# Optimization experiments

Measured on AMD Instinct MI355X. Metric: run time of the kernel, lower is better.

## Reference

```python
import jax, jax.numpy as jnp
import numpy as np

T, N, XD, H, Z, E = 6, 4096, 64, 256, 128, 131072


def setup_inputs() -> dict:
    key = jax.random.key(0)
    ks = jax.random.split(key, 16)
    f32 = jnp.float32
    def rn(k, shp):
        return jax.random.normal(k, shp, f32)
    def gl(k, shp):  # glorot-ish init, scaled by fan_in
        return jax.random.normal(k, shp, f32) * np.float32(1.0 / np.sqrt(shp[-2]))
    return {
        "x": rn(ks[0], (T, N, XD)),
        "edges": jax.random.randint(ks[1], (T, 2, E), 0, N, dtype=jnp.int32),
        "eps": rn(ks[2], (T, N, Z)),
        "drop_u": jax.random.uniform(ks[3], (T, N, Z), f32),
        "phi_x_w": gl(ks[4], (XD, H)), "phi_x_b": jnp.zeros((H,), f32),
        "phi_z_w": gl(ks[5], (Z, H)), "phi_z_b": jnp.zeros((H,), f32),
        "enc_w": gl(ks[6], (2 * H, H)),
        "enc_mu_w": gl(ks[7], (H, Z)),
        "enc_lv_w": gl(ks[8], (H, Z)),
        "prior_w": gl(ks[9], (H, H)), "prior_b": jnp.zeros((H,), f32),
        "prior_mu_w": gl(ks[10], (H, Z)), "prior_mu_b": jnp.zeros((Z,), f32),
        "prior_lv_w": gl(ks[11], (H, Z)), "prior_lv_b": jnp.zeros((Z,), f32),
        "gru_wx": gl(ks[12], (4, 2 * H, H)),  # gates i,f,o,c; x-side GCN weights
        "gru_wh": gl(ks[13], (4, H, H)),      # gates i,f,o,c; h-side GCN weights
    }


def reference(x, edges, eps, drop_u, phi_x_w, phi_x_b, phi_z_w, phi_z_b,
              enc_w, enc_mu_w, enc_lv_w, prior_w, prior_b,
              prior_mu_w, prior_mu_b, prior_lv_w, prior_lv_b,
              gru_wx, gru_wh):
    T_, N_, _ = x.shape
    H_ = phi_x_w.shape[1]
    h = jnp.zeros((N_, H_), x.dtype)
    c = jnp.zeros((N_, H_), x.dtype)
    loop = jnp.arange(N_, dtype=edges.dtype)
    enc_mus, prior_mus = [], []
    dec_t = None
    for t in range(T_):  # fixed small T; edge structure differs per step
        row = jnp.concatenate([edges[t, 0], loop])  # add self loops
        col = jnp.concatenate([edges[t, 1], loop])
        deg = jax.ops.segment_sum(jnp.ones(row.shape, x.dtype), row, num_segments=N_)
        dinv = jnp.where(deg > 0, jax.lax.rsqrt(deg), jnp.zeros((), x.dtype))
        norm = (dinv[row] * dinv[col])[:, None]

        def gcn(xx, W):
            # GCNConv: xW, gather at col, scale by sym-norm, scatter-add at row
            return jax.ops.segment_sum(norm * (xx @ W)[col], row, num_segments=N_)

        phi_x_t = jax.nn.relu(x[t] @ phi_x_w + phi_x_b)
        enc_t = jax.nn.relu(gcn(jnp.concatenate([phi_x_t, h], axis=1), enc_w))
        enc_mu_t = gcn(enc_t, enc_mu_w)
        enc_std_t = jax.nn.softplus(gcn(enc_t, enc_lv_w))
        prior_t = jax.nn.relu(h @ prior_w + prior_b)
        prior_mu_t = prior_t @ prior_mu_w + prior_mu_b
        _prior_std_t = jax.nn.softplus(prior_t @ prior_lv_w + prior_lv_b)  # computed as in original, unused in returns
        z_t = eps[t] * enc_std_t + enc_mu_t  # original: eps.mul(logvar).add_(mu)
        phi_z_t = jax.nn.relu(z_t @ phi_z_w + phi_z_b)
        # InnerProductDecoder with dropout(p=0.5, training=True), identity act
        z_drop = jnp.where(drop_u[t] < 0.5, z_t * 2.0, jnp.zeros((), x.dtype))
        dec_t = z_drop @ z_drop.T  # [N, N]
        # graph-LSTM step (n_layer = 1)
        xin = jnp.concatenate([phi_x_t, phi_z_t], axis=1)  # [N, 2H]
        gi = jax.nn.sigmoid(gcn(xin, gru_wx[0]) + gcn(h, gru_wh[0]))
        gf = jax.nn.sigmoid(gcn(xin, gru_wx[1]) + gcn(h, gru_wh[1]))
        go = jax.nn.sigmoid(gcn(xin, gru_wx[2]) + gcn(h, gru_wh[2]))
        ct = jnp.tanh(gcn(xin, gru_wx[3]) + gcn(h, gru_wh[3]))
        c_new = gf * h + gi * ct    # faithful to original: F_g * h[i] (not c)
        h_new = go * jnp.tanh(c)    # faithful to original: uses old c[i]
        h, c = h_new, c_new
        enc_mus.append(enc_mu_t)
        prior_mus.append(prior_mu_t)
    return jnp.stack(enc_mus), jnp.stack(prior_mus), h[None], dec_t
```

## Files before the change

### kernel.cpp

```cpp
#include <hip/hip_runtime.h>
#include <math.h>

#define T_  6
#define NN  4096
#define XD_ 64
#define H_  256
#define ZZ  128
#define EE  131072

typedef unsigned short u16;
typedef __attribute__((ext_vector_type(8))) short short8;
typedef __attribute__((ext_vector_type(8))) unsigned short u16x8;
typedef __attribute__((ext_vector_type(4))) float f32x4;

__device__ __forceinline__ float bf2f(u16 u) { return __uint_as_float(((unsigned)u) << 16); }
__device__ __forceinline__ u16 f2bf(float f) {
    unsigned x = __float_as_uint(f);
    return (u16)((x + 0x7FFFu + ((x >> 16) & 1u)) >> 16);
}

__global__ void k_deg(const int* __restrict__ edges, int* __restrict__ degcnt) {
    int t = blockIdx.y;
    int e = blockIdx.x * 256 + threadIdx.x;
    const int* rows = edges + (size_t)t * 2 * EE;
    atomicAdd(&degcnt[t * NN + rows[e]], 1);
}

__global__ void k_scan_dinv(const int* __restrict__ degcnt_all,
                            int* __restrict__ row_start_all,
                            int* __restrict__ cursor_all,
                            float* __restrict__ dinv_all) {
    __shared__ int sbuf[1024];
    int tt = blockIdx.x;
    const int* degcnt = degcnt_all + tt * NN;
    int* row_start = row_start_all + tt * (NN + 1);
    int* cursor = cursor_all + tt * NN;
    float* dinv = dinv_all + tt * NN;
    int t = threadIdx.x;
    int b = t * 4;
    int v0 = degcnt[b + 0], v1 = degcnt[b + 1], v2 = degcnt[b + 2], v3 = degcnt[b + 3];
    dinv[b + 0] = rsqrtf((float)(v0 + 1));
    dinv[b + 1] = rsqrtf((float)(v1 + 1));
    dinv[b + 2] = rsqrtf((float)(v2 + 1));
    dinv[b + 3] = rsqrtf((float)(v3 + 1));
    int s = v0 + v1 + v2 + v3;
    sbuf[t] = s;
    __syncthreads();
    for (int off = 1; off < 1024; off <<= 1) {
        int x = sbuf[t];
        int y = (t >= off) ? sbuf[t - off] : 0;
        __syncthreads();
        sbuf[t] = x + y;
        __syncthreads();
    }
    int excl = sbuf[t] - s;
    int r0 = excl, r1 = excl + v0, r2 = r1 + v1, r3 = r2 + v2;
    row_start[b + 0] = r0; cursor[b + 0] = r0;
    row_start[b + 1] = r1; cursor[b + 1] = r1;
    row_start[b + 2] = r2; cursor[b + 2] = r2;
    row_start[b + 3] = r3; cursor[b + 3] = r3;
    if (t == 1023) row_start[NN] = r3 + v3;
}

__global__ void k_scatter(const int* __restrict__ edges,
                          int* __restrict__ cursor, const float* __restrict__ dinv,
                          int* __restrict__ col_idx, float* __restrict__ val,
                          const float* __restrict__ pm0, float* __restrict__ out_pm) {
    int idx = blockIdx.x * 256 + threadIdx.x;
    if (idx < T_ * EE) {
        int t = idx >> 17, e = idx & (EE - 1);
        const int* rows = edges + (size_t)t * 2 * EE;
        const int* cols = rows + EE;
        int r = rows[e], cc = cols[e];
        int pos = atomicAdd(&cursor[t * NN + r], 1);
        col_idx[(size_t)t * EE + pos] = cc;
        val[(size_t)t * EE + pos] = dinv[t * NN + r] * dinv[t * NN + cc];
        return;
    }
    idx -= T_ * EE;
    if (idx < NN * ZZ / 4) {
        int j4 = idx & 31;
        ((float4*)out_pm)[idx] = *(const float4*)(pm0 + j4 * 4);
    }
}

__device__ __forceinline__ void sp_row_wave(const u16* __restrict__ Y,
                                            const int* __restrict__ row_start,
                                            const int* __restrict__ col_idx,
                                            const float* __restrict__ val,
                                            const float* __restrict__ dinv,
                                            u16* __restrict__ outp, int ldo, int r) {
    int lane = threadIdx.x & 63;
    int half = lane >> 5;
    int cg2 = lane & 31;
    int s0 = row_start[r], s1 = row_start[r + 1];
    float a[8] = {0.f, 0.f, 0.f, 0.f, 0.f, 0.f, 0.f, 0.f};
    for (int base = s0; base < s1; base += 64) {
        int n = s1 - base; if (n > 64) n = 64;
        int cl = 0; float vl = 0.f;
        if (base + lane < s1) { cl = col_idx[base + lane]; vl = val[base + lane]; }
        for (int e = 0; e < n; e += 8) {
            int e0 = e + half, e1 = e + 2 + half, e2 = e + 4 + half, e3 = e + 6 + half;
            int cc0 = __shfl(cl, e0);
            float v0 = (e0 < n) ? __shfl(vl, e0) : 0.f;
            int cc1 = __shfl(cl, e1);
            float v1 = (e1 < n) ? __shfl(vl, e1) : 0.f;
            int cc2 = __shfl(cl, e2);
            float v2 = (e2 < n) ? __shfl(vl, e2) : 0.f;
            int cc3 = __shfl(cl, e3);
            float v3 = (e3 < n) ? __shfl(vl, e3) : 0.f;
            u16x8 y0 = *(const u16x8*)(Y + (size_t)cc0 * H_ + cg2 * 8);
            u16x8 y1 = *(const u16x8*)(Y + (size_t)cc1 * H_ + cg2 * 8);
            u16x8 y2 = *(const u16x8*)(Y + (size_t)cc2 * H_ + cg2 * 8);
            u16x8 y3 = *(const u16x8*)(Y + (size_t)cc3 * H_ + cg2 * 8);
#pragma unroll
            for (int j = 0; j < 8; ++j) a[j] += v0 * bf2f(y0[j]);
#pragma unroll
            for (int j = 0; j < 8; ++j) a[j] += v1 * bf2f(y1[j]);
#pragma unroll
            for (int j = 0; j < 8; ++j) a[j] += v2 * bf2f(y2[j]);
#pragma unroll
            for (int j = 0; j < 8; ++j) a[j] += v3 * bf2f(y3[j]);
        }
    }
#pragma unroll
    for (int j = 0; j < 8; ++j) a[j] += __shfl_xor(a[j], 32);
    if (half == 0) {
        float dr = dinv[r], sc = dr * dr;
        u16x8 ys = *(const u16x8*)(Y + (size_t)r * H_ + cg2 * 8);
        u16x8 o;
#pragma unroll
        for (int j = 0; j < 8; ++j) o[j] = f2bf(a[j] + sc * bf2f(ys[j]));
        *(u16x8*)(outp + (size_t)r * ldo + cg2 * 8) = o;
    }
}

__global__ void k_spmm(const u16* __restrict__ Y1,
                       const int* __restrict__ row_start_all, const int* __restrict__ col_idx_all,
                       const float* __restrict__ val_all, const float* __restrict__ dinv_all,
                       u16* __restrict__ out1, int ldo,
                       long long sY, long long sO) {
    int t = blockIdx.y;
    int w = threadIdx.x >> 6;
    sp_row_wave(Y1 + (size_t)t * sY, row_start_all + (size_t)t * (NN + 1),
                col_idx_all + (size_t)t * EE, val_all + (size_t)t * EE,
                dinv_all + (size_t)t * NN, out1 + (size_t)t * sO, ldo,
                blockIdx.x * 4 + w);
}

template<int MF>
__device__ __forceinline__ void mm_core(const u16* __restrict__ A, int lda,
                                        const u16* __restrict__ BT, int ldbt, int K,
                                        int row0, int col0,
                                        f32x4 acc[MF][MF], char* smem) {
    constexpr int TILE = MF * 32;
    u16* As = (u16*)smem;
    u16* Bs = As + TILE * 64;
    const int lane = threadIdx.x & 63;
    const int w = threadIdx.x >> 6;
    const int wr = (w >> 1) * (TILE / 2);
    const int wc = (w & 1) * (TILE / 2);

    int gRow[MF], gCol[MF];
#pragma unroll
    for (int i = 0; i < MF; ++i) {
        int G = (w * MF + i) * 64 + lane;
        int r = G >> 3;
        gRow[i] = r;
        gCol[i] = ((G & 7) ^ (r & 7)) << 3;
    }

    for (int k0 = 0; k0 < K; k0 += 64) {
#pragma unroll
        for (int i = 0; i < MF; ++i) {
            const u16* sa = A + (size_t)(row0 + gRow[i]) * lda + k0 + gCol[i];
            __builtin_amdgcn_global_load_lds(
                (const __attribute__((address_space(1))) void*)sa,
                (__attribute__((address_space(3))) void*)(As + (w * MF + i) * 512), 16, 0, 0);
            const u16* sb = BT + (size_t)(col0 + gRow[i]) * ldbt + k0 + gCol[i];
            __builtin_amdgcn_global_load_lds(
                (const __attribute__((address_space(1))) void*)sb,
                (__attribute__((address_space(3))) void*)(Bs + (w * MF + i) * 512), 16, 0, 0);
        }
        __syncthreads();
#pragma unroll
        for (int kk = 0; kk < 2; ++kk) {
            short8 a[MF], b[MF];
#pragma unroll
            for (int mf = 0; mf < MF; ++mf) {
                int r = wr + mf * 16 + (lane & 15);
                int off = (r * 128 + kk * 64 + (lane >> 4) * 16) ^ ((r & 7) << 4);
                a[mf] = *(const short8*)((const char*)As + off);
            }
#pragma unroll
            for (int nf = 0; nf < MF; ++nf) {
                int r = wc + nf * 16 + (lane & 15);
                int off = (r * 128 + kk * 64 + (lane >> 4) * 16) ^ ((r & 7) << 4);
                b[nf] = *(const short8*)((const char*)Bs + off);
            }
#pragma unroll
            for (int mf = 0; mf < MF; ++mf)
#pragma unroll
                for (int nf = 0; nf < MF; ++nf)
                    acc[mf][nf] = __builtin_amdgcn_mfma_f32_16x16x32_bf16(
                        a[mf], b[nf], acc[mf][nf], 0, 0, 0);
        }
        __syncthreads();
    }
}

__device__ __forceinline__ void mm_core32(const u16* __restrict__ A, int lda,
                                          const u16* __restrict__ BT, int ldbt, int K,
                                          int row0, int col0,
                                          f32x4 acc[2], char* smem) {
    u16* As = (u16*)smem;
    u16* Bs = As + 32 * 64;
    const int lane = threadIdx.x & 63;
    const int w = threadIdx.x >> 6;
    const int wr = (w >> 1) * 16;
    const int wc = (w & 1) * 32;

    int aR, aC;
    { int G = w * 64 + lane; int r = G >> 3; aR = r; aC = ((G & 7) ^ (r & 7)) << 3; }
    int bR[2], bC[2];
#pragma unroll
    for (int i = 0; i < 2; ++i) {
        int G = (w * 2 + i) * 64 + lane; int r = G >> 3;
        bR[i] = r; bC[i] = ((G & 7) ^ (r & 7)) << 3;
    }

    for (int k0 = 0; k0 < K; k0 += 64) {
        const u16* sa = A + (size_t)(row0 + aR) * lda + k0 + aC;
        __builtin_amdgcn_global_load_lds(
            (const __attribute__((address_space(1))) void*)sa,
            (__attribute__((address_space(3))) void*)(As + w * 512), 16, 0, 0);
#pragma unroll
        for (int i = 0; i < 2; ++i) {
            const u16* sb = BT + (size_t)(col0 + bR[i]) * ldbt + k0 + bC[i];
            __builtin_amdgcn_global_load_lds(
                (const __attribute__((address_space(1))) void*)sb,
                (__attribute__((address_space(3))) void*)(Bs + (w * 2 + i) * 512), 16, 0, 0);
        }
        __syncthreads();
#pragma unroll
        for (int kk = 0; kk < 2; ++kk) {
            short8 a, b[2];
            {
                int r = wr + (lane & 15);
                int off = (r * 128 + kk * 64 + (lane >> 4) * 16) ^ ((r & 7) << 4);
                a = *(const short8*)((const char*)As + off);
            }
#pragma unroll
            for (int nf = 0; nf < 2; ++nf) {
                int r = wc + nf * 16 + (lane & 15);
                int off = (r * 128 + kk * 64 + (lane >> 4) * 16) ^ ((r & 7) << 4);
                b[nf] = *(const short8*)((const char*)Bs + off);
            }
            acc[0] = __builtin_amdgcn_mfma_f32_16x16x32_bf16(a, b[0], acc[0], 0, 0, 0);
            acc[1] = __builtin_amdgcn_mfma_f32_16x16x32_bf16(a, b[1], acc[1], 0, 0, 0);
        }
        __syncthreads();
    }
}

__device__ __forceinline__ void zacc2(f32x4 acc[2][2]) {
#pragma unroll
    for (int i = 0; i < 2; ++i)
#pragma unroll
        for (int j = 0; j < 2; ++j) acc[i][j] = f32x4{0.f, 0.f, 0.f, 0.f};
}

__device__ __forceinline__ void epi_bf16relu(f32x4 acc[2][2], u16* __restrict__ C,
                                             int ldc, int row0, int col0,
                                             const float* __restrict__ bias) {
    const int lane = threadIdx.x & 63, w = threadIdx.x >> 6;
    const int wr = (w >> 1) * 32, wc = (w & 1) * 32;
    const int ci = lane & 15, ri = (lane >> 4) * 4;
#pragma unroll
    for (int mf = 0; mf < 2; ++mf)
#pragma unroll
        for (int nf = 0; nf < 2; ++nf) {
            int row = row0 + wr + mf * 16 + ri;
            int col = col0 + wc + nf * 16 + ci;
            float bv = bias ? bias[col] : 0.f;
#pragma unroll
            for (int i = 0; i < 4; ++i)
                C[(size_t)(row + i) * ldc + col] = f2bf(fmaxf(acc[mf][nf][i] + bv, 0.f));
        }
}

__device__ __forceinline__ void epi32_bf16relu(f32x4 acc[2], u16* __restrict__ C,
                                               int ldc, int row0, int col0,
                                               const float* __restrict__ bias) {
    const int lane = threadIdx.x & 63, w = threadIdx.x >> 6;
    const int wr = (w >> 1) * 16, wc = (w & 1) * 32;
    const int ci = lane & 15, ri = (lane >> 4) * 4;
#pragma unroll
    for (int nf = 0; nf < 2; ++nf) {
        int row = row0 + wr + ri;
        int col = col0 + wc + nf * 16 + ci;
        float bv = bias ? bias[col] : 0.f;
#pragma unroll
        for (int i = 0; i < 4; ++i)
            C[(size_t)(row + i) * ldc + col] = f2bf(fmaxf(acc[nf][i] + bv, 0.f));
    }
}

__device__ __forceinline__ void epi_f32b(f32x4 acc[2][2], float* __restrict__ C,
                                         int ldc, int row0, int col0,
                                         const float* __restrict__ bias) {
    const int lane = threadIdx.x & 63, w = threadIdx.x >> 6;
    const int wr = (w >> 1) * 32, wc = (w & 1) * 32;
    const int ci = lane & 15, ri = (lane >> 4) * 4;
#pragma unroll
    for (int mf = 0; mf < 2; ++mf)
#pragma unroll
        for (int nf = 0; nf < 2; ++nf) {
            int row = row0 + wr + mf * 16 + ri;
            int col = col0 + wc + nf * 16 + ci;
            float bv = bias[col];
#pragma unroll
            for (int i = 0; i < 4; ++i)
                C[(size_t)(row + i) * ldc + col] = acc[mf][nf][i] + bv;
        }
}

template<int MF>
__launch_bounds__(256)
__global__ void k_mm(const u16* __restrict__ A, int lda,
                     const u16* __restrict__ BT, int ldbt, int K,
                     float* __restrict__ C0, int ldc0,
                     u16* __restrict__ C1, int ldc1,
                     const float* __restrict__ bias, int act) {
    constexpr int TILE = MF * 32;
    __shared__ alignas(16) char smem[TILE * 64 * 4];

    const int lane = threadIdx.x & 63;
    const int w = threadIdx.x >> 6;
    const int row0 = blockIdx.y * TILE;
    const int col0 = blockIdx.x * TILE;
    const int wr = (w >> 1) * (TILE / 2);
    const int wc = (w & 1) * (TILE / 2);

    f32x4 acc[MF][MF];
#pragma unroll
    for (int i = 0; i < MF; ++i)
#pragma unroll
        for (int j = 0; j < MF; ++j)
            acc[i][j] = f32x4{0.f, 0.f, 0.f, 0.f};

    mm_core<MF>(A, lda, BT, ldbt, K, row0, col0, acc, smem);

    const int ci = lane & 15;
    const int ri = (lane >> 4) * 4;
#pragma unroll
    for (int mf = 0; mf < MF; ++mf) {
#pragma unroll
        for (int nf = 0; nf < MF; ++nf) {
            int row = row0 + wr + mf * 16 + ri;
            int col = col0 + wc + nf * 16 + ci;
            if (C1) {
                float bv = bias ? bias[col] : 0.f;
#pragma unroll
                for (int i = 0; i < 4; ++i) {
                    float v = acc[mf][nf][i] + bv;
                    if (act == 1) v = fmaxf(v, 0.f);
                    C1[(size_t)(row + i) * ldc1 + col] = f2bf(v);
                }
            } else {
                float bv = bias ? bias[col] : 0.f;
#pragma unroll
                for (int i = 0; i < 4; ++i)
                    C0[(size_t)(row + i) * ldc0 + col] = acc[mf][nf][i] + bv;
            }
        }
    }
}

__launch_bounds__(256)
__global__ void k_mm32(const u16* __restrict__ A, int lda,
                       const u16* __restrict__ BT, int ldbt, int K,
                       float* __restrict__ C0,
                       u16* __restrict__ C1, int ldc1,
                       const float* __restrict__ bias, int act,
                       const float* __restrict__ eps,
                       const float* __restrict__ du, u16* __restrict__ zdOut) {
    __shared__ alignas(16) char smem[12288];
    const int tid = threadIdx.x;
    const int lane = tid & 63;
    const int w = tid >> 6;
    const int row0 = blockIdx.y * 32;
    const int col0 = blockIdx.x * 64;

    f32x4 acc[2];
    acc[0] = f32x4{0.f, 0.f, 0.f, 0.f};
    acc[1] = f32x4{0.f, 0.f, 0.f, 0.f};
    mm_core32(A, lda, BT, ldbt, K, row0, col0, acc, smem);

    if (act == 1) {
        epi32_bf16relu(acc, C1, ldc1, row0, col0, bias);
        return;
    }
    const int wr = (w >> 1) * 16, wc = (w & 1) * 32;
    const int ci = lane & 15, ri = (lane >> 4) * 4;
    float (*epi)[68] = (float(*)[68])smem;
#pragma unroll
    for (int nf = 0; nf < 2; ++nf)
#pragma unroll
        for (int i = 0; i < 4; ++i)
            epi[wr + ri + i][wc + nf * 16 + ci] = acc[nf][i];
    __syncthreads();
#pragma unroll
    for (int k = 0; k < 4; ++k) {
        int p = tid + k * 256;
        int row = p >> 5, jl = p & 31;
        float mu = epi[row][jl * 2];
        float sp = epi[row][jl * 2 + 1];
        float sd = (sp > 20.f) ? sp : log1pf(expf(sp));
        int idx = (row0 + row) * ZZ + (col0 >> 1) + jl;
        C0[idx] = mu;
        u16 z16 = f2bf(eps[idx] * sd + mu);
        C1[idx] = z16;
        if (zdOut)
            zdOut[idx] = (du[idx] < 0.5f) ? f2bf(2.f * bf2f(z16)) : (u16)0;
    }
}

__launch_bounds__(256)
__global__ void k_dual32(const u16* __restrict__ A0, int lda0, const u16* __restrict__ BT0,
                         int ldbt0, int K0, u16* __restrict__ Cb0, int ldcb0,
                         const u16* __restrict__ A1, int lda1, const u16* __restrict__ BT1,
                         int ldbt1, int K1, float* __restrict__ Cf1, int ldcf1,
                         const float* __restrict__ bias1) {
    __shared__ alignas(16) char smem[16384];
    if (blockIdx.z == 0) {
        const int row0 = blockIdx.y * 32;
        const int col0 = blockIdx.x * 64;
        f32x4 acc[2];
        acc[0] = f32x4{0.f, 0.f, 0.f, 0.f};
        acc[1] = f32x4{0.f, 0.f, 0.f, 0.f};
        mm_core32(A0, lda0, BT0, ldbt0, K0, row0, col0, acc, smem);
        epi32_bf16relu(acc, Cb0, ldcb0, row0, col0, nullptr);
    } else {
        if (blockIdx.x >= 2 || blockIdx.y >= 64) return;
        const int row0 = blockIdx.y * 64;
        const int col0 = blockIdx.x * 64;
        f32x4 acc[2][2]; zacc2(acc);
        mm_core<2>(A1, lda1, BT1, ldbt1, K1, row0, col0, acc, smem);
        epi_f32b(acc, Cf1, ldcf1, row0, col0, bias1);
    }
}

__launch_bounds__(256)
__global__ void k_sp_mm(const u16* __restrict__ Y, const int* __restrict__ row_start,
                        const int* __restrict__ col_idx, const float* __restrict__ val,
                        const float* __restrict__ dinv, u16* __restrict__ spOut, int spLdo,
                        int doSp,
                        const u16* __restrict__ A, int lda, const u16* __restrict__ BT,
                        int ldbt, int K, u16* __restrict__ Cb, int ldcb,
                        const float* __restrict__ bias, int gx) {
    __shared__ alignas(16) char smem[16384];
    int bid = blockIdx.x;
    if (bid < NN / 4) {
        if (!doSp) return;
        int w = threadIdx.x >> 6;
        sp_row_wave(Y, row_start, col_idx, val, dinv, spOut, spLdo, bid * 4 + w);
        return;
    }
    int b2 = bid - NN / 4;
    const int row0 = (b2 / gx) * 64;
    const int col0 = (b2 % gx) * 64;
    f32x4 acc[2][2]; zacc2(acc);
    mm_core<2>(A, lda, BT, ldbt, K, row0, col0, acc, smem);
    epi_bf16relu(acc, Cb, ldcb, row0, col0, bias);
}

__launch_bounds__(256)
__global__ void k_gates(const u16* __restrict__ XIN, const u16* __restrict__ BgT,
                        float* __restrict__ h, float* __restrict__ c,
                        u16* __restrict__ hbf, float* __restrict__ hOut,
                        int skipSH) {
    __shared__ alignas(16) char smem[34816];
    u16* As = (u16*)smem;
    u16* Bs = As + 128 * 64;
    const int tid = threadIdx.x;
    const int lane = tid & 63;
    const int w = tid >> 6;
    const int row0 = blockIdx.y * 128;
    const int col0 = blockIdx.x * 64;
    const int wrB = (w >> 1) * 64;
    const int wc = (w & 1) * 32;

    f32x4 acc[4][2];
#pragma unroll
    for (int i = 0; i < 4; ++i)
#pragma unroll
        for (int j = 0; j < 2; ++j) acc[i][j] = f32x4{0.f, 0.f, 0.f, 0.f};

    int aRow[4], aCol[4];
#pragma unroll
    for (int i = 0; i < 4; ++i) {
        int G = (w * 4 + i) * 64 + lane;
        int r = G >> 3;
        aRow[i] = r;
        aCol[i] = ((G & 7) ^ (r & 7)) << 3;
    }
    int bRow[2], bCol[2];
#pragma unroll
    for (int i = 0; i < 2; ++i) {
        int G = (w * 2 + i) * 64 + lane;
        int r = G >> 3;
        bRow[i] = r;
        bCol[i] = ((G & 7) ^ (r & 7)) << 3;
    }

    const int nIter = skipSH ? 8 : 12;
    for (int it = 0; it < nIter; ++it) {
        int k0 = it * 64 + ((skipSH && it >= 4) ? 256 : 0);
#pragma unroll
        for (int i = 0; i < 4; ++i) {
            const u16* sa = XIN + (size_t)(row0 + aRow[i]) * 768 + k0 + aCol[i];
            __builtin_amdgcn_global_load_lds(
                (const __attribute__((address_space(1))) void*)sa,
                (__attribute__((address_space(3))) void*)(As + (w * 4 + i) * 512), 16, 0, 0);
        }
#pragma unroll
        for (int i = 0; i < 2; ++i) {
            const u16* sb = BgT + (size_t)(col0 + bRow[i]) * 768 + k0 + bCol[i];
            __builtin_amdgcn_global_load_lds(
                (const __attribute__((address_space(1))) void*)sb,
                (__attribute__((address_space(3))) void*)(Bs + (w * 2 + i) * 512), 16, 0, 0);
        }
        __syncthreads();
#pragma unroll
        for (int kk = 0; kk < 2; ++kk) {
            short8 a[4], b[2];
#pragma unroll
            for (int mf = 0; mf < 4; ++mf) {
                int r = wrB + mf * 16 + (lane & 15);
                int off = (r * 128 + kk * 64 + (lane >> 4) * 16) ^ ((r & 7) << 4);
                a[mf] = *(const short8*)((const char*)As + off);
            }
#pragma unroll
            for (int nf = 0; nf < 2; ++nf) {
                int r = wc + nf * 16 + (lane & 15);
                int off = (r * 128 + kk * 64 + (lane >> 4) * 16) ^ ((r & 7) << 4);
                b[nf] = *(const short8*)((const char*)Bs + off);
            }
#pragma unroll
            for (int mf = 0; mf < 4; ++mf)
#pragma unroll
                for (int nf = 0; nf < 2; ++nf)
                    acc[mf][nf] = __builtin_amdgcn_mfma_f32_16x16x32_bf16(
                        a[mf], b[nf], acc[mf][nf], 0, 0, 0);
        }
        __syncthreads();
    }

    const int ci = lane & 15;
    const int ri = (lane >> 4) * 4;
    float (*epi)[68] = (float(*)[68])smem;
#pragma unroll
    for (int mf = 0; mf < 4; ++mf)
#pragma unroll
        for (int nf = 0; nf < 2; ++nf)
#pragma unroll
            for (int i = 0; i < 4; ++i)
                epi[wrB + mf * 16 + ri + i][wc + nf * 16 + ci] = acc[mf][nf][i];
    __syncthreads();
#pragma unroll
    for (int k = 0; k < 8; ++k) {
        int p = tid + k * 256;
        int row = p >> 4, jl = p & 15;
        float4 g4 = *(const float4*)&epi[row][jl * 4];
        float gi = 1.f / (1.f + expf(-g4.x));
        float gf = 1.f / (1.f + expf(-g4.y));
        float go = 1.f / (1.f + expf(-g4.z));
        float ct = tanhf(g4.w);
        int idx = (row0 + row) * H_ + (col0 >> 2) + jl;
        float ho = h[idx], co = c[idx];
        float cn = gf * ho + gi * ct;
        float hn = go * tanhf(co);
        h[idx] = hn;
        c[idx] = cn;
        hbf[idx] = f2bf(hn);
        if (hOut) hOut[idx] = hn;
    }
}

__global__ void k_prep(const float* __restrict__ phi_x_w, const float* __restrict__ phi_z_w,
                       const float* __restrict__ enc_w, const float* __restrict__ prior_w,
                       const float* __restrict__ prior_mu_w,
                       const float* __restrict__ enc_mu_w, const float* __restrict__ enc_lv_w,
                       const float* __restrict__ gru_wx, const float* __restrict__ gru_wh,
                       u16* __restrict__ phi_x_wT, u16* __restrict__ phi_z_wT,
                       u16* __restrict__ enc_wT, u16* __restrict__ prior_wT,
                       u16* __restrict__ prior_mu_wT, u16* __restrict__ mulvT,
                       u16* __restrict__ BgT,
                       const float* __restrict__ x, u16* __restrict__ x_bf,
                       int* __restrict__ degcnt,
                       const float* __restrict__ prior_b,
                       const float* __restrict__ prior_mu_b,
                       float* __restrict__ pm0,
                       float4* __restrict__ hcz) {
    int idx = blockIdx.x * 256 + threadIdx.x;
    if (idx < 16384) {
        int j = idx >> 6, k = idx & 63;
        phi_x_wT[idx] = f2bf(phi_x_w[k * 256 + j]);
        return;
    }
    idx -= 16384;
    if (idx < 32768) {
        int j = idx >> 7, k = idx & 127;
        phi_z_wT[idx] = f2bf(phi_z_w[k * 256 + j]);
        return;
    }
    idx -= 32768;
    if (idx < 131072) {
        int j = idx >> 9, k = idx & 511;
        enc_wT[idx] = f2bf(enc_w[k * 256 + j]);
        return;
    }
    idx -= 131072;
    if (idx < 65536) {
        int j = idx >> 8, k = idx & 255;
        prior_wT[idx] = f2bf(prior_w[k * 256 + j]);
        return;
    }
    idx -= 65536;
    if (idx < 32768) {
        int j = idx >> 8, k = idx & 255;
        prior_mu_wT[idx] = f2bf(prior_mu_w[k * 128 + j]);
        return;
    }
    idx -= 32768;
    if (idx < 65536) {
        int cp = idx >> 8, k = idx & 255;
        int j = cp >> 1, s = cp & 1;
        float v = s ? enc_lv_w[k * 128 + j] : enc_mu_w[k * 128 + j];
        mulvT[idx] = f2bf(v);
        return;
    }
    idx -= 65536;
    if (idx < 786432) {
        int cp = idx / 768, k = idx % 768;
        int g = cp & 3, j = cp >> 2;
        float v;
        if (k < 256)      v = gru_wx[((size_t)g * 512 + k) * 256 + j];
        else if (k < 512) v = gru_wh[((size_t)g * 256 + (k - 256)) * 256 + j];
        else              v = gru_wx[((size_t)g * 512 + (k - 256)) * 256 + j];
        BgT[idx] = f2bf(v);
        return;
    }
    idx -= 786432;
    if (idx < 393216) {
        float4 v = ((const float4*)x)[idx];
        ((ushort4*)x_bf)[idx] = make_ushort4(f2bf(v.x), f2bf(v.y), f2bf(v.z), f2bf(v.w));
        return;
    }
    idx -= 393216;
    if (idx < 6144) {
        ((int4*)degcnt)[idx] = make_int4(0, 0, 0, 0);
        return;
    }
    idx -= 6144;
    if (idx < 128) {
        float acc = prior_mu_b[idx];
        for (int k = 0; k < 256; ++k) {
            float pt = bf2f(f2bf(fmaxf(prior_b[k], 0.f)));
            acc += pt * bf2f(f2bf(prior_mu_w[k * 128 + idx]));
        }
        pm0[idx] = acc;
        return;
    }
    idx -= 128;
    if (idx < 655360)
        hcz[idx] = make_float4(0.f, 0.f, 0.f, 0.f);
}

extern "C" void kernel_launch(void* const* d_in, const int* in_sizes, int n_in,
                              void* d_out_v, int out_size, void* d_ws, size_t ws_size,
                              hipStream_t stream) {
    (void)in_sizes; (void)n_in; (void)out_size;
    const float* x          = (const float*)d_in[0];
    const int*   edges      = (const int*)d_in[1];
    const float* eps        = (const float*)d_in[2];
    const float* drop_u     = (const float*)d_in[3];
    const float* phi_x_w    = (const float*)d_in[4];
    const float* phi_x_b    = (const float*)d_in[5];
    const float* phi_z_w    = (const float*)d_in[6];
    const float* phi_z_b    = (const float*)d_in[7];
    const float* enc_w      = (const float*)d_in[8];
    const float* enc_mu_w   = (const float*)d_in[9];
    const float* enc_lv_w   = (const float*)d_in[10];
    const float* prior_w    = (const float*)d_in[11];
    const float* prior_b    = (const float*)d_in[12];
    const float* prior_mu_w = (const float*)d_in[13];
    const float* prior_mu_b = (const float*)d_in[14];
    const float* gru_wx     = (const float*)d_in[17];
    const float* gru_wh     = (const float*)d_in[18];
    float* out = (float*)d_out_v;

    char* base = (char*)d_ws;
    size_t cur = 0;
    auto carve = [&](size_t bytes) -> void* {
        void* p = base + cur;
        cur += (bytes + 255) & ~(size_t)255;
        return p;
    };
    float* h         = (float*)carve((size_t)NN * H_ * 4);
    float* c         = (float*)carve((size_t)NN * H_ * 4);
    u16* h_bf        = (u16*)carve((size_t)NN * H_ * 2);
    float* dinv      = (float*)carve((size_t)T_ * NN * 4);
    int*   degcnt    = (int*)carve((size_t)T_ * NN * 4);
    int*   row_start = (int*)carve((size_t)T_ * (NN + 1) * 4);
    int*   cursor    = (int*)carve((size_t)T_ * NN * 4);
    int*   col_idx   = (int*)carve((size_t)T_ * EE * 4);
    float* val       = (float*)carve((size_t)T_ * EE * 4);
    u16* x_bf        = (u16*)carve((size_t)T_ * NN * XD_ * 2);
    u16* phi6        = (u16*)carve((size_t)T_ * NN * H_ * 2);
    u16* phiz        = (u16*)carve((size_t)NN * H_ * 2);
    u16* enc_t       = (u16*)carve((size_t)NN * H_ * 2);
    u16* SEb         = (u16*)carve((size_t)NN * H_ * 2);
    u16* prior_t     = (u16*)carve((size_t)NN * H_ * 2);
    u16* XIN6        = (u16*)carve((size_t)T_ * NN * 768 * 2);
    u16* zbuf        = (u16*)carve((size_t)NN * ZZ * 2);
    u16* zd          = (u16*)carve((size_t)NN * ZZ * 2);
    u16* phi_x_wT    = (u16*)carve((size_t)XD_ * H_ * 2);
    u16* phi_z_wT    = (u16*)carve((size_t)ZZ * H_ * 2);
    u16* enc_wT      = (u16*)carve((size_t)512 * H_ * 2);
    u16* prior_wT    = (u16*)carve((size_t)H_ * H_ * 2);
    u16* prior_mu_wT = (u16*)carve((size_t)ZZ * H_ * 2);
    u16* mulvT       = (u16*)carve((size_t)H_ * H_ * 2);
    u16* BgT         = (u16*)carve((size_t)1024 * 768 * 2);
    float* pm0       = (float*)carve(128 * 4);
    if (cur > ws_size) return;

    const size_t NZ = (size_t)NN * ZZ;
    const size_t HOFF = (size_t)2 * T_ * NZ;
    const size_t DECOFF = HOFF + (size_t)NN * H_;

    k_prep<<<(2185344 + 255) / 256, 256, 0, stream>>>(
        phi_x_w, phi_z_w, enc_w, prior_w, prior_mu_w, enc_mu_w, enc_lv_w,
        gru_wx, gru_wh,
        phi_x_wT, phi_z_wT, enc_wT, prior_wT, prior_mu_wT, mulvT, BgT,
        x, x_bf, degcnt, prior_b, prior_mu_b, pm0, (float4*)h);
    k_deg<<<dim3(EE / 256, T_), 256, 0, stream>>>(edges, degcnt);
    k_scan_dinv<<<T_, 1024, 0, stream>>>(degcnt, row_start, cursor, dinv);
    k_scatter<<<(T_ * EE + NN * ZZ / 4 + 255) / 256, 256, 0, stream>>>(
        edges, cursor, dinv, col_idx, val, pm0, out + (size_t)T_ * NZ);
    k_mm<2><<<dim3(4, (T_ * NN) / 64), 256, 0, stream>>>(x_bf, XD_, phi_x_wT, XD_, XD_,
        nullptr, 0, phi6, H_, phi_x_b, 1);
    k_spmm<<<dim3(NN / 4, T_), 256, 0, stream>>>(phi6, row_start, col_idx, val, dinv,
        XIN6, 768, (long long)NN * H_, (long long)NN * 768);

    for (int t = 0; t < T_; ++t) {
        const int* rs_t = row_start + (size_t)t * (NN + 1);
        const int* ci_t = col_idx + (size_t)t * EE;
        const float* vv_t = val + (size_t)t * EE;
        const float* dv_t = dinv + (size_t)t * NN;
        u16* xin_t = XIN6 + (size_t)t * NN * 768;
        int last = (t == T_ - 1);

        if (t > 0)
            k_sp_mm<<<NN / 4 + 256, 256, 0, stream>>>(h_bf, rs_t, ci_t, vv_t, dv_t,
                xin_t + 256, 768, 1,
                h_bf, H_, prior_wT, H_, H_, prior_t, H_, prior_b, 4);
        k_dual32<<<dim3(4, 128, (t == 0) ? 1 : 2), 256, 0, stream>>>(
            xin_t, 768, enc_wT, 512, (t == 0) ? 256 : 512, enc_t, H_,
            prior_t, H_, prior_mu_wT, H_, H_,
            out + (size_t)(T_ + t) * NZ, ZZ, prior_mu_b);
        k_spmm<<<dim3(NN / 4, 1), 256, 0, stream>>>(enc_t, rs_t, ci_t, vv_t, dv_t,
                                                    SEb, H_, 0, 0);
        k_mm32<<<dim3(4, 128), 256, 0, stream>>>(SEb, H_, mulvT, H_, H_,
            out + (size_t)t * NZ, zbuf, ZZ, nullptr, 4,
            eps + (size_t)t * NZ,
            last ? drop_u + (size_t)t * NZ : nullptr, last ? zd : nullptr);
        k_mm32<<<dim3(4, 128), 256, 0, stream>>>(zbuf, ZZ, phi_z_wT, ZZ, ZZ,
            nullptr, phiz, H_, phi_z_b, 1, nullptr, nullptr, nullptr);
        k_spmm<<<dim3(NN / 4, 1), 256, 0, stream>>>(phiz, rs_t, ci_t, vv_t, dv_t,
                                                    xin_t + 512, 768, 0, 0);
        k_gates<<<dim3(16, 32), 256, 0, stream>>>(xin_t, BgT, h, c, h_bf,
            last ? out + HOFF : nullptr, t == 0);
    }

    k_mm<4><<<dim3(32, 32), 256, 0, stream>>>(zd, ZZ, zd, ZZ, ZZ,
        out + DECOFF, NN, nullptr, 0, nullptr, 0);
}
```

Baseline: 537.0 us.

## Interleave CSR column and value into int2 and load edges directly per lane

Packs each CSR entry's column index and normalisation weight into one int2 array, replacing the two separate arrays. The SpMM row kernel now has each lane load its own (col,val) pairs directly from memory instead of loading a 64-entry chunk cooperatively and broadcasting with shuffles. The aim is to remove the shuffle overhead and the per-chunk loop, at the cost of redundant cached loads of the same entries across lanes and a clamped-index load for the row tail.

New measurement: 563.7 us. +5.0%, slower.

```diff
diff --git a/kernel.cpp b/kernel.cpp
--- a/kernel.cpp
+++ b/kernel.cpp
@@ -64,7 +64,7 @@
 
 __global__ void k_scatter(const int* __restrict__ edges,
                           int* __restrict__ cursor, const float* __restrict__ dinv,
-                          int* __restrict__ col_idx, float* __restrict__ val,
+                          int2* __restrict__ cv,
                           const float* __restrict__ pm0, float* __restrict__ out_pm) {
     int idx = blockIdx.x * 256 + threadIdx.x;
     if (idx < T_ * EE) {
@@ -73,8 +73,8 @@
         const int* cols = rows + EE;
         int r = rows[e], cc = cols[e];
         int pos = atomicAdd(&cursor[t * NN + r], 1);
-        col_idx[(size_t)t * EE + pos] = cc;
-        val[(size_t)t * EE + pos] = dinv[t * NN + r] * dinv[t * NN + cc];
+        float v = dinv[t * NN + r] * dinv[t * NN + cc];
+        cv[(size_t)t * EE + pos] = make_int2(cc, __float_as_int(v));
         return;
     }
     idx -= T_ * EE;
@@ -86,8 +86,7 @@
 
 __device__ __forceinline__ void sp_row_wave(const u16* __restrict__ Y,
                                             const int* __restrict__ row_start,
-                                            const int* __restrict__ col_idx,
-                                            const float* __restrict__ val,
+                                            const int2* __restrict__ cv,
                                             const float* __restrict__ dinv,
                                             u16* __restrict__ outp, int ldo, int r) {
     int lane = threadIdx.x & 63;
@@ -95,33 +94,29 @@
     int cg2 = lane & 31;
     int s0 = row_start[r], s1 = row_start[r + 1];
     float a[8] = {0.f, 0.f, 0.f, 0.f, 0.f, 0.f, 0.f, 0.f};
-    for (int base = s0; base < s1; base += 64) {
-        int n = s1 - base; if (n > 64) n = 64;
-        int cl = 0; float vl = 0.f;
-        if (base + lane < s1) { cl = col_idx[base + lane]; vl = val[base + lane]; }
-        for (int e = 0; e < n; e += 8) {
-            int e0 = e + half, e1 = e + 2 + half, e2 = e + 4 + half, e3 = e + 6 + half;
-            int cc0 = __shfl(cl, e0);
-            float v0 = (e0 < n) ? __shfl(vl, e0) : 0.f;
-            int cc1 = __shfl(cl, e1);
-            float v1 = (e1 < n) ? __shfl(vl, e1) : 0.f;
-            int cc2 = __shfl(cl, e2);
-            float v2 = (e2 < n) ? __shfl(vl, e2) : 0.f;
-            int cc3 = __shfl(cl, e3);
-            float v3 = (e3 < n) ? __shfl(vl, e3) : 0.f;
-            u16x8 y0 = *(const u16x8*)(Y + (size_t)cc0 * H_ + cg2 * 8);
-            u16x8 y1 = *(const u16x8*)(Y + (size_t)cc1 * H_ + cg2 * 8);
-            u16x8 y2 = *(const u16x8*)(Y + (size_t)cc2 * H_ + cg2 * 8);
-            u16x8 y3 = *(const u16x8*)(Y + (size_t)cc3 * H_ + cg2 * 8);
-#pragma unroll
-            for (int j = 0; j < 8; ++j) a[j] += v0 * bf2f(y0[j]);
-#pragma unroll
-            for (int j = 0; j < 8; ++j) a[j] += v1 * bf2f(y1[j]);
-#pragma unroll
-            for (int j = 0; j < 8; ++j) a[j] += v2 * bf2f(y2[j]);
-#pragma unroll
-            for (int j = 0; j < 8; ++j) a[j] += v3 * bf2f(y3[j]);
-        }
+    for (int e = s0; e < s1; e += 8) {
+        int e0 = e + half, e1 = e + 2 + half, e2 = e + 4 + half, e3 = e + 6 + half;
+        int lim = s1 - 1;
+        int2 c0 = cv[min(e0, lim)];
+        int2 c1 = cv[min(e1, lim)];
+        int2 c2 = cv[min(e2, lim)];
+        int2 c3 = cv[min(e3, lim)];
+        u16x8 y0 = *(const u16x8*)(Y + (size_t)c0.x * H_ + cg2 * 8);
+        u16x8 y1 = *(const u16x8*)(Y + (size_t)c1.x * H_ + cg2 * 8);
+        u16x8 y2 = *(const u16x8*)(Y + (size_t)c2.x * H_ + cg2 * 8);
+        u16x8 y3 = *(const u16x8*)(Y + (size_t)c3.x * H_ + cg2 * 8);
+        float v0 = (e0 < s1) ? __int_as_float(c0.y) : 0.f;
+        float v1 = (e1 < s1) ? __int_as_float(c1.y) : 0.f;
+        float v2 = (e2 < s1) ? __int_as_float(c2.y) : 0.f;
+        float v3 = (e3 < s1) ? __int_as_float(c3.y) : 0.f;
+#pragma unroll
+        for (int j = 0; j < 8; ++j) a[j] += v0 * bf2f(y0[j]);
+#pragma unroll
+        for (int j = 0; j < 8; ++j) a[j] += v1 * bf2f(y1[j]);
+#pragma unroll
+        for (int j = 0; j < 8; ++j) a[j] += v2 * bf2f(y2[j]);
+#pragma unroll
+        for (int j = 0; j < 8; ++j) a[j] += v3 * bf2f(y3[j]);
     }
 #pragma unroll
     for (int j = 0; j < 8; ++j) a[j] += __shfl_xor(a[j], 32);
@@ -136,14 +131,14 @@
 }
 
 __global__ void k_spmm(const u16* __restrict__ Y1,
-                       const int* __restrict__ row_start_all, const int* __restrict__ col_idx_all,
-                       const float* __restrict__ val_all, const float* __restrict__ dinv_all,
+                       const int* __restrict__ row_start_all, const int2* __restrict__ cv_all,
+                       const float* __restrict__ dinv_all,
                        u16* __restrict__ out1, int ldo,
                        long long sY, long long sO) {
     int t = blockIdx.y;
     int w = threadIdx.x >> 6;
     sp_row_wave(Y1 + (size_t)t * sY, row_start_all + (size_t)t * (NN + 1),
-                col_idx_all + (size_t)t * EE, val_all + (size_t)t * EE,
+                cv_all + (size_t)t * EE,
                 dinv_all + (size_t)t * NN, out1 + (size_t)t * sO, ldo,
                 blockIdx.x * 4 + w);
 }
@@ -453,7 +448,7 @@
 
 __launch_bounds__(256)
 __global__ void k_sp_mm(const u16* __restrict__ Y, const int* __restrict__ row_start,
-                        const int* __restrict__ col_idx, const float* __restrict__ val,
+                        const int2* __restrict__ cv,
                         const float* __restrict__ dinv, u16* __restrict__ spOut, int spLdo,
                         int doSp,
                         const u16* __restrict__ A, int lda, const u16* __restrict__ BT,
@@ -464,7 +459,7 @@
     if (bid < NN / 4) {
         if (!doSp) return;
         int w = threadIdx.x >> 6;
-        sp_row_wave(Y, row_start, col_idx, val, dinv, spOut, spLdo, bid * 4 + w);
+        sp_row_wave(Y, row_start, cv, dinv, spOut, spLdo, bid * 4 + w);
         return;
     }
     int b2 = bid - NN / 4;
@@ -715,8 +710,7 @@
     int*   degcnt    = (int*)carve((size_t)T_ * NN * 4);
     int*   row_start = (int*)carve((size_t)T_ * (NN + 1) * 4);
     int*   cursor    = (int*)carve((size_t)T_ * NN * 4);
-    int*   col_idx   = (int*)carve((size_t)T_ * EE * 4);
-    float* val       = (float*)carve((size_t)T_ * EE * 4);
+    int2*  cv        = (int2*)carve((size_t)T_ * EE * 8);
     u16* x_bf        = (u16*)carve((size_t)T_ * NN * XD_ * 2);
     u16* phi6        = (u16*)carve((size_t)T_ * NN * H_ * 2);
     u16* phiz        = (u16*)carve((size_t)NN * H_ * 2);
@@ -748,29 +742,28 @@
     k_deg<<<dim3(EE / 256, T_), 256, 0, stream>>>(edges, degcnt);
     k_scan_dinv<<<T_, 1024, 0, stream>>>(degcnt, row_start, cursor, dinv);
     k_scatter<<<(T_ * EE + NN * ZZ / 4 + 255) / 256, 256, 0, stream>>>(
-        edges, cursor, dinv, col_idx, val, pm0, out + (size_t)T_ * NZ);
+        edges, cursor, dinv, cv, pm0, out + (size_t)T_ * NZ);
     k_mm<2><<<dim3(4, (T_ * NN) / 64), 256, 0, stream>>>(x_bf, XD_, phi_x_wT, XD_, XD_,
         nullptr, 0, phi6, H_, phi_x_b, 1);
-    k_spmm<<<dim3(NN / 4, T_), 256, 0, stream>>>(phi6, row_start, col_idx, val, dinv,
+    k_spmm<<<dim3(NN / 4, T_), 256, 0, stream>>>(phi6, row_start, cv, dinv,
         XIN6, 768, (long long)NN * H_, (long long)NN * 768);
 
     for (int t = 0; t < T_; ++t) {
         const int* rs_t = row_start + (size_t)t * (NN + 1);
-        const int* ci_t = col_idx + (size_t)t * EE;
-        const float* vv_t = val + (size_t)t * EE;
+        const int2* cv_t = cv + (size_t)t * EE;
         const float* dv_t = dinv + (size_t)t * NN;
         u16* xin_t = XIN6 + (size_t)t * NN * 768;
         int last = (t == T_ - 1);
 
         if (t > 0)
-            k_sp_mm<<<NN / 4 + 256, 256, 0, stream>>>(h_bf, rs_t, ci_t, vv_t, dv_t,
+            k_sp_mm<<<NN / 4 + 256, 256, 0, stream>>>(h_bf, rs_t, cv_t, dv_t,
                 xin_t + 256, 768, 1,
                 h_bf, H_, prior_wT, H_, H_, prior_t, H_, prior_b, 4);
         k_dual32<<<dim3(4, 128, (t == 0) ? 1 : 2), 256, 0, stream>>>(
             xin_t, 768, enc_wT, 512, (t == 0) ? 256 : 512, enc_t, H_,
             prior_t, H_, prior_mu_wT, H_, H_,
             out + (size_t)(T_ + t) * NZ, ZZ, prior_mu_b);
-        k_spmm<<<dim3(NN / 4, 1), 256, 0, stream>>>(enc_t, rs_t, ci_t, vv_t, dv_t,
+        k_spmm<<<dim3(NN / 4, 1), 256, 0, stream>>>(enc_t, rs_t, cv_t, dv_t,
                                                     SEb, H_, 0, 0);
         k_mm32<<<dim3(4, 128), 256, 0, stream>>>(SEb, H_, mulvT, H_, H_,
             out + (size_t)t * NZ, zbuf, ZZ, nullptr, 4,
@@ -778,7 +771,7 @@
             last ? drop_u + (size_t)t * NZ : nullptr, last ? zd : nullptr);
         k_mm32<<<dim3(4, 128), 256, 0, stream>>>(zbuf, ZZ, phi_z_wT, ZZ, ZZ,
             nullptr, phiz, H_, phi_z_b, 1, nullptr, nullptr, nullptr);
-        k_spmm<<<dim3(NN / 4, 1), 256, 0, stream>>>(phiz, rs_t, ci_t, vv_t, dv_t,
+        k_spmm<<<dim3(NN / 4, 1), 256, 0, stream>>>(phiz, rs_t, cv_t, dv_t,
                                                     xin_t + 512, 768, 0, 0);
         k_gates<<<dim3(16, 32), 256, 0, stream>>>(xin_t, BgT, h, c, h_bf,
             last ? out + HOFF : nullptr, t == 0);
```
